# Kernel tuning notes

Measured on AMD Instinct MI355X. Metric: run time of the kernel, lower is better.

The kernel has to match this reference:

```python
import jax, jax.numpy as jnp
import numpy as np

N = 200000   # nodes
E = 6400000  # edges (avg degree 32)
F_IN = 128
N_CLASSES = 4
DIMS = [F_IN, 24, 12, 6, 4, 2]


def setup_inputs() -> dict:
    key = jax.random.key(0)
    ks = jax.random.split(key, 16)
    inp = {}
    inp['x'] = jax.random.normal(ks[0], (N, F_IN), dtype=jnp.float32)
    inp['edge_index'] = jax.random.randint(ks[1], (2, E), 0, N, dtype=jnp.int32)
    for i in range(5):
        fan_in = DIMS[i]
        inp[f'W{i+1}'] = jax.random.normal(ks[2 + i], (DIMS[i], DIMS[i + 1]), dtype=jnp.float32) / np.float32(np.sqrt(fan_in))
        inp[f'b{i+1}'] = jnp.zeros((DIMS[i + 1],), dtype=jnp.float32)
    inp['Wc'] = jax.random.normal(ks[8], (2, N_CLASSES), dtype=jnp.float32) / np.float32(np.sqrt(2.0))
    inp['bc'] = jnp.zeros((N_CLASSES,), dtype=jnp.float32)
    return inp


def _gcn_forward(x, row, col, norm, weights, biases, Wc, bc):
    h = x
    for W, b in zip(weights, biases):
        xl = h @ W                               # [N, d_out] linear transform first (d_out <= d_in)
        msg = norm[:, None] * xl[row]            # gather + normalize: [E+N, d_out]
        agg = jax.ops.segment_max(msg, col, num_segments=N)  # aggr='max'
        h = jnp.tanh(agg + b)
    out = h @ Wc + bc
    return out, h


def reference(x, edge_index, W1, b1, W2, b2, W3, b3, W4, b4, W5, b5, Wc, bc):
    loops = jnp.arange(N, dtype=edge_index.dtype)
    row = jnp.concatenate([edge_index[0], loops])  # source (with self loops)
    col = jnp.concatenate([edge_index[1], loops])  # target
    # symmetric GCN normalization on A + I
    deg = jax.ops.segment_sum(jnp.ones_like(col, dtype=jnp.float32), col, num_segments=N)
    dinv = jnp.where(deg > 0, jax.lax.rsqrt(deg), 0.0)
    norm = dinv[row] * dinv[col]                   # [E+N]
    weights = [W1, W2, W3, W4, W5]
    biases = [b1, b2, b3, b4, b5]
    return _gcn_forward(x, row, col, norm, weights, biases, Wc, bc)
```

## Files before the change

### kernel.cpp

```cpp
#include <hip/hip_runtime.h>
#include <cmath>

#define NN 200000
#define EE 6400000
#define NBKT 391
#define GRID_A 512
#define BLK_A 256
#define RB_SHIFT 13
#define NRB 25

__device__ __forceinline__ unsigned int fenc(float f) {
    unsigned int u = __float_as_uint(f);
    return (u & 0x80000000u) ? ~u : (u | 0x80000000u);
}
__device__ __forceinline__ float fdec(unsigned int u) {
    unsigned int v = (u & 0x80000000u) ? (u & 0x7FFFFFFFu) : ~u;
    return __uint_as_float(v);
}


__global__ __launch_bounds__(BLK_A) void count_buckets_kernel(const int* __restrict__ col,
                                                              int* __restrict__ blkhist) {
    __shared__ int h[NBKT];
    for (int t = threadIdx.x; t < NBKT; t += BLK_A) h[t] = 0;
    __syncthreads();
    const int4* col4 = (const int4*)col;
    for (int i = blockIdx.x * BLK_A + threadIdx.x; i < EE / 4; i += GRID_A * BLK_A) {
        int4 c = col4[i];
        atomicAdd(&h[c.x >> 9], 1);
        atomicAdd(&h[c.y >> 9], 1);
        atomicAdd(&h[c.z >> 9], 1);
        atomicAdd(&h[c.w >> 9], 1);
    }
    __syncthreads();
    for (int t = threadIdx.x; t < NBKT; t += BLK_A) blkhist[blockIdx.x * NBKT + t] = h[t];
}

__global__ __launch_bounds__(GRID_A) void scan_cols_kernel(int* __restrict__ blkhist,
                                                           int* __restrict__ btot) {
    __shared__ int sc[GRID_A];
    int bkt = blockIdx.x, t = threadIdx.x;
    int v = blkhist[t * NBKT + bkt];
    sc[t] = v;
    __syncthreads();
    for (int off = 1; off < GRID_A; off <<= 1) {
        int add = (t >= off) ? sc[t - off] : 0;
        __syncthreads();
        sc[t] += add;
        __syncthreads();
    }
    blkhist[t * NBKT + bkt] = sc[t] - v;
    if (t == GRID_A - 1) btot[bkt] = sc[t];
}

__global__ __launch_bounds__(512) void scan_btot_kernel(const int* __restrict__ btot,
                                                        int* __restrict__ bbase) {
    __shared__ int sc[512];
    int t = threadIdx.x;
    int v = (t < NBKT) ? btot[t] : 0;
    sc[t] = v;
    __syncthreads();
    for (int off = 1; off < 512; off <<= 1) {
        int add = (t >= off) ? sc[t - off] : 0;
        __syncthreads();
        sc[t] += add;
        __syncthreads();
    }
    if (t < NBKT) bbase[t] = sc[t] - v;
    if (t == NBKT - 1) bbase[NBKT] = sc[t];
}

__global__ __launch_bounds__(BLK_A) void place_pairs_kernel(const int* __restrict__ row,
                                                            const int* __restrict__ col,
                                                            const int* __restrict__ blkhist,
                                                            const int* __restrict__ bbase,
                                                            unsigned int* __restrict__ pairs) {
    __shared__ int cur[NBKT];
    for (int t = threadIdx.x; t < NBKT; t += BLK_A)
        cur[t] = bbase[t] + blkhist[blockIdx.x * NBKT + t];
    __syncthreads();
    const int4* col4 = (const int4*)col;
    const int4* row4 = (const int4*)row;
    for (int i = blockIdx.x * BLK_A + threadIdx.x; i < EE / 4; i += GRID_A * BLK_A) {
        int4 c = col4[i];
        int4 r = row4[i];
        int p0 = atomicAdd(&cur[c.x >> 9], 1);
        pairs[p0] = (unsigned int)r.x | ((unsigned int)(c.x & 511) << 18);
        int p1 = atomicAdd(&cur[c.y >> 9], 1);
        pairs[p1] = (unsigned int)r.y | ((unsigned int)(c.y & 511) << 18);
        int p2 = atomicAdd(&cur[c.z >> 9], 1);
        pairs[p2] = (unsigned int)r.z | ((unsigned int)(c.z & 511) << 18);
        int p3 = atomicAdd(&cur[c.w >> 9], 1);
        pairs[p3] = (unsigned int)r.w | ((unsigned int)(c.w & 511) << 18);
    }
}

__global__ __launch_bounds__(512) void bucket_build_band_kernel(const unsigned int* __restrict__ pairs,
                                                                const int* __restrict__ bbase,
                                                                float* __restrict__ dinv,
                                                                unsigned int* __restrict__ codes,
                                                                int* __restrict__ bandoffs) {
    __shared__ int bin[512 * NRB];
    __shared__ int sc[512];
    int b = blockIdx.x, tid = threadIdx.x;
    int base = bbase[b], end = bbase[b + 1];
    int node0 = b << 9;
    int nloc = NN - node0; if (nloc > 512) nloc = 512;

    for (int t = tid; t < 512 * NRB; t += 512) bin[t] = 0;
    __syncthreads();
    for (int i = base + tid; i < end; i += 512) {
        unsigned int p = pairs[i];
        int lc = p >> 18;
        int rw = (int)(p & 0x3FFFFu);
        atomicAdd(&bin[(rw >> RB_SHIFT) * 512 + lc], 1);
    }
    __syncthreads();

    if (tid < nloc) {
        int d = 0;
#pragma unroll
        for (int bb = 0; bb < NRB; ++bb) d += bin[bb * 512 + tid];
        dinv[node0 + tid] = rsqrtf((float)(d + 1));
    }
    __syncthreads();

    int tot = 0;
#pragma unroll
    for (int i = 0; i < NRB; ++i) tot += bin[tid * NRB + i];
    sc[tid] = tot;
    __syncthreads();
    for (int off = 1; off < 512; off <<= 1) {
        int add = (tid >= off) ? sc[tid - off] : 0;
        __syncthreads();
        sc[tid] += add;
        __syncthreads();
    }
    int run = base + sc[tid] - tot;
#pragma unroll
    for (int i = 0; i < NRB; ++i) {
        int c = bin[tid * NRB + i];
        bin[tid * NRB + i] = run;
        run += c;
    }
    __syncthreads();

    if (tid < NRB) bandoffs[b * (NRB + 1) + tid] = bin[tid * 512];
    if (tid == 0) bandoffs[b * (NRB + 1) + NRB] = end;
    __syncthreads();

    for (int i = base + tid; i < end; i += 512) {
        unsigned int p = pairs[i];
        int lc = p >> 18;
        int rw = (int)(p & 0x3FFFFu);
        int pos = atomicAdd(&bin[(rw >> RB_SHIFT) * 512 + lc], 1);
        codes[pos] = p;
    }
}

__global__ void matmul128_y_kernel(const float* __restrict__ x, const float* __restrict__ W,
                                   const float* __restrict__ dinv, float* __restrict__ y, int n) {
    __shared__ float Ws[128 * 24];
    for (int t = threadIdx.x; t < 128 * 24; t += blockDim.x) Ws[t] = W[t];
    __syncthreads();
    int i = blockIdx.x * blockDim.x + threadIdx.x;
    if (i >= n) return;
    float acc[24];
#pragma unroll
    for (int j = 0; j < 24; ++j) acc[j] = 0.f;
    const float4* hr = (const float4*)(x + (size_t)i * 128);
#pragma unroll 8
    for (int k4 = 0; k4 < 32; ++k4) {
        float4 hv = hr[k4];
        const float* wk = &Ws[k4 * 4 * 24];
#pragma unroll
        for (int j = 0; j < 24; ++j) acc[j] += hv.x * wk[j];
#pragma unroll
        for (int j = 0; j < 24; ++j) acc[j] += hv.y * wk[24 + j];
#pragma unroll
        for (int j = 0; j < 24; ++j) acc[j] += hv.z * wk[48 + j];
#pragma unroll
        for (int j = 0; j < 24; ++j) acc[j] += hv.w * wk[72 + j];
    }
    float di = dinv[i];
    float4* orow = (float4*)(y + (size_t)i * 24);
#pragma unroll
    for (int q = 0; q < 6; ++q) {
        float4 o;
        o.x = di * acc[q * 4 + 0];
        o.y = di * acc[q * 4 + 1];
        o.z = di * acc[q * 4 + 2];
        o.w = di * acc[q * 4 + 3];
        orow[q] = o;
    }
}

template<int DOUT, int DNEXT, bool FINAL>
__global__ __launch_bounds__(512) void gather_band_kernel(const unsigned int* __restrict__ codes,
                                                          const int* __restrict__ bandoffs,
                                                          const float* __restrict__ dinv,
                                                          const float* __restrict__ y,
                                                          const float* __restrict__ bias,
                                                          const float* __restrict__ Wn,
                                                          const float* __restrict__ bcls,
                                                          float* __restrict__ outp,
                                                          float* __restrict__ hout) {
    constexpr int ST = DOUT + 1;
    __shared__ unsigned int acc[512 * ST];
    __shared__ float dcs[512];
    __shared__ float Ws[DOUT * DNEXT];
    __shared__ float bs[DOUT];
    const int b0 = blockIdx.x;
    const int node0 = b0 << 9;
    const int nloc = (NN - node0 < 512) ? (NN - node0) : 512;
    const int tid = threadIdx.x;

    if (tid < DOUT * DNEXT) Ws[tid] = Wn[tid];
    if (tid < DOUT) bs[tid] = bias[tid];
    if (tid < nloc) dcs[tid] = dinv[node0 + tid];
    for (int idx = tid; idx < nloc * DOUT; idx += 512) {
        int lc = idx / DOUT;
        int f  = idx - lc * DOUT;
        acc[lc * ST + f] = fenc(y[(size_t)node0 * DOUT + idx]);
    }
    __syncthreads();

    const int* bo = bandoffs + b0 * (NRB + 1);
#pragma unroll 1
    for (int bb = 0; bb < NRB; ++bb) {
        const int e = bo[bb + 1];
        for (int i = bo[bb] + tid; i < e; i += 512) {
            unsigned int p = codes[i];
            int lc = (int)(p >> 18);
            size_t r = (size_t)(p & 0x3FFFFu);
            unsigned int* a = &acc[lc * ST];
            if constexpr (DOUT % 4 == 0) {
                const float4* yr = (const float4*)(y + r * DOUT);
                float4 c[DOUT / 4];
#pragma unroll
                for (int q = 0; q < DOUT / 4; ++q) c[q] = yr[q];
#pragma unroll
                for (int q = 0; q < DOUT / 4; ++q) {
                    unsigned int e0 = fenc(c[q].x), e1 = fenc(c[q].y);
                    unsigned int e2 = fenc(c[q].z), e3 = fenc(c[q].w);
                    if (e0 > a[q * 4 + 0]) atomicMax(&a[q * 4 + 0], e0);
                    if (e1 > a[q * 4 + 1]) atomicMax(&a[q * 4 + 1], e1);
                    if (e2 > a[q * 4 + 2]) atomicMax(&a[q * 4 + 2], e2);
                    if (e3 > a[q * 4 + 3]) atomicMax(&a[q * 4 + 3], e3);
                }
            } else {
                const float2* yr = (const float2*)(y + r * DOUT);
                float2 c[DOUT / 2];
#pragma unroll
                for (int q = 0; q < DOUT / 2; ++q) c[q] = yr[q];
#pragma unroll
                for (int q = 0; q < DOUT / 2; ++q) {
                    unsigned int e0 = fenc(c[q].x), e1 = fenc(c[q].y);
                    if (e0 > a[q * 2 + 0]) atomicMax(&a[q * 2 + 0], e0);
                    if (e1 > a[q * 2 + 1]) atomicMax(&a[q * 2 + 1], e1);
                }
            }
        }
        __syncthreads();
    }

    float* hsf = (float*)acc;
    for (int idx = tid; idx < nloc * DOUT; idx += 512) {
        int lc = idx / DOUT;
        int f  = idx - lc * DOUT;
        hsf[lc * ST + f] = tanhf(dcs[lc] * fdec(acc[lc * ST + f]) + bs[f]);
    }
    __syncthreads();

    if constexpr (!FINAL) {
        for (int idx = tid; idx < nloc * DNEXT; idx += 512) {
            int lc = idx / DNEXT;
            int j = idx - lc * DNEXT;
            float a = 0.f;
#pragma unroll
            for (int k = 0; k < DOUT; ++k) a += hsf[lc * ST + k] * Ws[k * DNEXT + j];
            outp[(size_t)node0 * DNEXT + idx] = dcs[lc] * a;
        }
    } else {
        for (int lc = tid; lc < nloc; lc += 512) {
            float h0 = hsf[lc * ST], h1 = hsf[lc * ST + 1];
            float2 ho; ho.x = h0; ho.y = h1;
            ((float2*)hout)[node0 + lc] = ho;
            float4 o;
            o.x = h0 * Ws[0] + h1 * Ws[DNEXT + 0] + bcls[0];
            o.y = h0 * Ws[1] + h1 * Ws[DNEXT + 1] + bcls[1];
            o.z = h0 * Ws[2] + h1 * Ws[DNEXT + 2] + bcls[2];
            o.w = h0 * Ws[3] + h1 * Ws[DNEXT + 3] + bcls[3];
            ((float4*)outp)[node0 + lc] = o;
        }
    }
}

extern "C" void kernel_launch(void* const* d_in, const int* in_sizes, int n_in,
                              void* d_out, int out_size, void* d_ws, size_t ws_size,
                              hipStream_t stream) {
    const float* x  = (const float*)d_in[0];
    const int*   ei = (const int*)d_in[1];
    const int* row = ei;
    const int* col = ei + EE;
    const float* W1 = (const float*)d_in[2];  const float* b1 = (const float*)d_in[3];
    const float* W2 = (const float*)d_in[4];  const float* b2 = (const float*)d_in[5];
    const float* W3 = (const float*)d_in[6];  const float* b3 = (const float*)d_in[7];
    const float* W4 = (const float*)d_in[8];  const float* b4 = (const float*)d_in[9];
    const float* W5 = (const float*)d_in[10]; const float* b5 = (const float*)d_in[11];
    const float* Wc = (const float*)d_in[12]; const float* bc = (const float*)d_in[13];
    float* out = (float*)d_out;

    char* ws = (char*)d_ws;
    float*        dinv       = (float*)(ws + 0);
    int*          bandoffs   = (int*)(ws + 800000);
    int*          bbase      = (int*)(ws + 840960);
    int*          btot       = (int*)(ws + 843008);
    int*          blkhist    = (int*)(ws + 845056);
    unsigned int* codes      = (unsigned int*)(ws + 1647872);
    unsigned int* pairs      = (unsigned int*)(ws + 27247872);
    float*        bufB       = (float*)(ws + 27247872);
    float*        bufA       = (float*)(ws + 52847872);

    const int BLK = 256;
    const int gN = (NN + BLK - 1) / BLK;

    count_buckets_kernel<<<GRID_A, BLK_A, 0, stream>>>(col, blkhist);
    scan_cols_kernel<<<NBKT, GRID_A, 0, stream>>>(blkhist, btot);
    scan_btot_kernel<<<1, 512, 0, stream>>>(btot, bbase);
    place_pairs_kernel<<<GRID_A, BLK_A, 0, stream>>>(row, col, blkhist, bbase, pairs);
    bucket_build_band_kernel<<<NBKT, 512, 0, stream>>>(pairs, bbase, dinv, codes, bandoffs);

    matmul128_y_kernel<<<gN, BLK, 0, stream>>>(x, W1, dinv, bufB, NN);

    gather_band_kernel<24, 12, false><<<NBKT, 512, 0, stream>>>(
        codes, bandoffs, dinv, bufB, b1, W2, nullptr, bufA, nullptr);
    gather_band_kernel<12, 6, false><<<NBKT, 512, 0, stream>>>(
        codes, bandoffs, dinv, bufA, b2, W3, nullptr, bufB, nullptr);
    gather_band_kernel<6, 4, false><<<NBKT, 512, 0, stream>>>(
        codes, bandoffs, dinv, bufB, b3, W4, nullptr, bufA, nullptr);
    gather_band_kernel<4, 2, false><<<NBKT, 512, 0, stream>>>(
        codes, bandoffs, dinv, bufA, b4, W5, nullptr, bufB, nullptr);
    gather_band_kernel<2, 4, true><<<NBKT, 512, 0, stream>>>(
        codes, bandoffs, dinv, bufB, b5, Wc, bc, out, out + (size_t)NN * 4);
}
```

Before: 722.6 us.

## Pre-encode features as ordered uints, unroll gather by two, widen row bands

Producers now write features already converted to the order-preserving unsigned encoding, so the gather loop no longer calls fenc per edge and issues atomicMax without the compare-before-atomic check. The gather loop handles two edges per thread per iteration so the loads for both are in flight together. The row-band shift goes from 13 to 14 (NRB 25 to 13), giving fewer band passes and block barriers at the cost of less locality of source rows within each band. Dropping the check means every edge now issues an LDS atomic, which adds atomic traffic that the early-out used to avoid.

```diff
diff --git a/kernel.cpp b/kernel.cpp
--- a/kernel.cpp
+++ b/kernel.cpp
@@ -6,8 +6,8 @@
 #define NBKT 391
 #define GRID_A 512
 #define BLK_A 256
-#define RB_SHIFT 13
-#define NRB 25
+#define RB_SHIFT 14
+#define NRB 13
 
 __device__ __forceinline__ unsigned int fenc(float f) {
     unsigned int u = __float_as_uint(f);
@@ -159,7 +159,7 @@
 }
 
 __global__ void matmul128_y_kernel(const float* __restrict__ x, const float* __restrict__ W,
-                                   const float* __restrict__ dinv, float* __restrict__ y, int n) {
+                                   const float* __restrict__ dinv, unsigned int* __restrict__ y, int n) {
     __shared__ float Ws[128 * 24];
     for (int t = threadIdx.x; t < 128 * 24; t += blockDim.x) Ws[t] = W[t];
     __syncthreads();
@@ -183,14 +183,14 @@
         for (int j = 0; j < 24; ++j) acc[j] += hv.w * wk[72 + j];
     }
     float di = dinv[i];
-    float4* orow = (float4*)(y + (size_t)i * 24);
+    uint4* orow = (uint4*)(y + (size_t)i * 24);
 #pragma unroll
     for (int q = 0; q < 6; ++q) {
-        float4 o;
-        o.x = di * acc[q * 4 + 0];
-        o.y = di * acc[q * 4 + 1];
-        o.z = di * acc[q * 4 + 2];
-        o.w = di * acc[q * 4 + 3];
+        uint4 o;
+        o.x = fenc(di * acc[q * 4 + 0]);
+        o.y = fenc(di * acc[q * 4 + 1]);
+        o.z = fenc(di * acc[q * 4 + 2]);
+        o.w = fenc(di * acc[q * 4 + 3]);
         orow[q] = o;
     }
 }
@@ -199,7 +199,7 @@
 __global__ __launch_bounds__(512) void gather_band_kernel(const unsigned int* __restrict__ codes,
                                                           const int* __restrict__ bandoffs,
                                                           const float* __restrict__ dinv,
-                                                          const float* __restrict__ y,
+                                                          const unsigned int* __restrict__ y,
                                                           const float* __restrict__ bias,
                                                           const float* __restrict__ Wn,
                                                           const float* __restrict__ bcls,
@@ -221,7 +221,7 @@
     for (int idx = tid; idx < nloc * DOUT; idx += 512) {
         int lc = idx / DOUT;
         int f  = idx - lc * DOUT;
-        acc[lc * ST + f] = fenc(y[(size_t)node0 * DOUT + idx]);
+        acc[lc * ST + f] = y[(size_t)node0 * DOUT + idx];
     }
     __syncthreads();
 
@@ -229,35 +229,71 @@
 #pragma unroll 1
     for (int bb = 0; bb < NRB; ++bb) {
         const int e = bo[bb + 1];
-        for (int i = bo[bb] + tid; i < e; i += 512) {
-            unsigned int p = codes[i];
-            int lc = (int)(p >> 18);
-            size_t r = (size_t)(p & 0x3FFFFu);
-            unsigned int* a = &acc[lc * ST];
+        for (int i = bo[bb] + tid; i < e; i += 1024) {
+            const int i2 = i + 512;
+            const bool two = (i2 < e);
+            unsigned int p0 = codes[i];
+            int lc0 = (int)(p0 >> 18);
+            size_t r0 = (size_t)(p0 & 0x3FFFFu);
+            unsigned int* a0 = &acc[lc0 * ST];
+            unsigned int p1 = 0; unsigned int* a1 = nullptr;
             if constexpr (DOUT % 4 == 0) {
-                const float4* yr = (const float4*)(y + r * DOUT);
-                float4 c[DOUT / 4];
-#pragma unroll
-                for (int q = 0; q < DOUT / 4; ++q) c[q] = yr[q];
-#pragma unroll
-                for (int q = 0; q < DOUT / 4; ++q) {
-                    unsigned int e0 = fenc(c[q].x), e1 = fenc(c[q].y);
-                    unsigned int e2 = fenc(c[q].z), e3 = fenc(c[q].w);
-                    if (e0 > a[q * 4 + 0]) atomicMax(&a[q * 4 + 0], e0);
-                    if (e1 > a[q * 4 + 1]) atomicMax(&a[q * 4 + 1], e1);
-                    if (e2 > a[q * 4 + 2]) atomicMax(&a[q * 4 + 2], e2);
-                    if (e3 > a[q * 4 + 3]) atomicMax(&a[q * 4 + 3], e3);
+                constexpr int NQ = DOUT / 4;
+                const uint4* y0 = (const uint4*)(y + r0 * DOUT);
+                uint4 c0[NQ];
+#pragma unroll
+                for (int q = 0; q < NQ; ++q) c0[q] = y0[q];
+                uint4 c1[NQ];
+                if (two) {
+                    p1 = codes[i2];
+                    size_t r1 = (size_t)(p1 & 0x3FFFFu);
+                    const uint4* y1 = (const uint4*)(y + r1 * DOUT);
+#pragma unroll
+                    for (int q = 0; q < NQ; ++q) c1[q] = y1[q];
+                    a1 = &acc[(p1 >> 18) * ST];
+                }
+#pragma unroll
+                for (int q = 0; q < NQ; ++q) {
+                    atomicMax(&a0[q * 4 + 0], c0[q].x);
+                    atomicMax(&a0[q * 4 + 1], c0[q].y);
+                    atomicMax(&a0[q * 4 + 2], c0[q].z);
+                    atomicMax(&a0[q * 4 + 3], c0[q].w);
+                }
+                if (two) {
+#pragma unroll
+                    for (int q = 0; q < NQ; ++q) {
+                        atomicMax(&a1[q * 4 + 0], c1[q].x);
+                        atomicMax(&a1[q * 4 + 1], c1[q].y);
+                        atomicMax(&a1[q * 4 + 2], c1[q].z);
+                        atomicMax(&a1[q * 4 + 3], c1[q].w);
+                    }
                 }
             } else {
-                const float2* yr = (const float2*)(y + r * DOUT);
-                float2 c[DOUT / 2];
-#pragma unroll
-                for (int q = 0; q < DOUT / 2; ++q) c[q] = yr[q];
-#pragma unroll
-                for (int q = 0; q < DOUT / 2; ++q) {
-                    unsigned int e0 = fenc(c[q].x), e1 = fenc(c[q].y);
-                    if (e0 > a[q * 2 + 0]) atomicMax(&a[q * 2 + 0], e0);
-                    if (e1 > a[q * 2 + 1]) atomicMax(&a[q * 2 + 1], e1);
+                constexpr int NQ = DOUT / 2;
+                const uint2* y0 = (const uint2*)(y + r0 * DOUT);
+                uint2 c0[NQ];
+#pragma unroll
+                for (int q = 0; q < NQ; ++q) c0[q] = y0[q];
+                uint2 c1[NQ];
+                if (two) {
+                    p1 = codes[i2];
+                    size_t r1 = (size_t)(p1 & 0x3FFFFu);
+                    const uint2* y1 = (const uint2*)(y + r1 * DOUT);
+#pragma unroll
+                    for (int q = 0; q < NQ; ++q) c1[q] = y1[q];
+                    a1 = &acc[(p1 >> 18) * ST];
+                }
+#pragma unroll
+                for (int q = 0; q < NQ; ++q) {
+                    atomicMax(&a0[q * 2 + 0], c0[q].x);
+                    atomicMax(&a0[q * 2 + 1], c0[q].y);
+                }
+                if (two) {
+#pragma unroll
+                    for (int q = 0; q < NQ; ++q) {
+                        atomicMax(&a1[q * 2 + 0], c1[q].x);
+                        atomicMax(&a1[q * 2 + 1], c1[q].y);
+                    }
                 }
             }
         }
@@ -273,13 +309,14 @@
     __syncthreads();
 
     if constexpr (!FINAL) {
+        unsigned int* outu = (unsigned int*)outp;
         for (int idx = tid; idx < nloc * DNEXT; idx += 512) {
             int lc = idx / DNEXT;
             int j = idx - lc * DNEXT;
             float a = 0.f;
 #pragma unroll
             for (int k = 0; k < DOUT; ++k) a += hsf[lc * ST + k] * Ws[k * DNEXT + j];
-            outp[(size_t)node0 * DNEXT + idx] = dcs[lc] * a;
+            outu[(size_t)node0 * DNEXT + idx] = fenc(dcs[lc] * a);
         }
     } else {
         for (int lc = tid; lc < nloc; lc += 512) {
@@ -319,8 +356,8 @@
     int*          blkhist    = (int*)(ws + 845056);
     unsigned int* codes      = (unsigned int*)(ws + 1647872);
     unsigned int* pairs      = (unsigned int*)(ws + 27247872);
-    float*        bufB       = (float*)(ws + 27247872);
-    float*        bufA       = (float*)(ws + 52847872);
+    unsigned int* bufB       = (unsigned int*)(ws + 27247872);
+    unsigned int* bufA       = (unsigned int*)(ws + 52847872);
 
     const int BLK = 256;
     const int gN = (NN + BLK - 1) / BLK;
@@ -334,13 +371,13 @@
     matmul128_y_kernel<<<gN, BLK, 0, stream>>>(x, W1, dinv, bufB, NN);
 
     gather_band_kernel<24, 12, false><<<NBKT, 512, 0, stream>>>(
-        codes, bandoffs, dinv, bufB, b1, W2, nullptr, bufA, nullptr);
+        codes, bandoffs, dinv, bufB, b1, W2, nullptr, (float*)bufA, nullptr);
     gather_band_kernel<12, 6, false><<<NBKT, 512, 0, stream>>>(
-        codes, bandoffs, dinv, bufA, b2, W3, nullptr, bufB, nullptr);
+        codes, bandoffs, dinv, bufA, b2, W3, nullptr, (float*)bufB, nullptr);
     gather_band_kernel<6, 4, false><<<NBKT, 512, 0, stream>>>(
-        codes, bandoffs, dinv, bufB, b3, W4, nullptr, bufA, nullptr);
+        codes, bandoffs, dinv, bufB, b3, W4, nullptr, (float*)bufA, nullptr);
     gather_band_kernel<4, 2, false><<<NBKT, 512, 0, stream>>>(
-        codes, bandoffs, dinv, bufA, b4, W5, nullptr, bufB, nullptr);
+        codes, bandoffs, dinv, bufA, b4, W5, nullptr, (float*)bufB, nullptr);
     gather_band_kernel<2, 4, true><<<NBKT, 512, 0, stream>>>(
         codes, bandoffs, dinv, bufB, b5, Wc, bc, out, out + (size_t)NN * 4);
 }
```

After: 742.2 us. 1.03x slower.
